# Performance work log

Measured on AMD Instinct MI355X. Metric: run time of the kernel, lower is better.

Reference implementation:

```python
import jax, jax.numpy as jnp
import numpy as np

B, M, N, P, H, W, D, DIMG, NH = 32, 2048, 512, 16, 640, 640, 256, 384, 8
PD = 3 * P * P  # 768 flattened patch dim


def layer_norm(x, g, b, eps=1e-5):
    mu = x.mean(-1, keepdims=True)
    var = ((x - mu) ** 2).mean(-1, keepdims=True)
    return (x - mu) * jax.lax.rsqrt(var + eps) * g + b


def get_patches(img, kpts, patch):
    # img [B,3,H,W], kpts [B,N,2] (x,y), NaN rows -> NaN patches
    Bb, C, Hh, Ww = img.shape
    half = patch // 2
    safe = jnp.nan_to_num(kpts, nan=0.0)
    ctr = jnp.round(safe).astype(jnp.int32)
    x0 = jnp.clip(ctr[..., 0] - half, 0, Ww - patch)
    y0 = jnp.clip(ctr[..., 1] - half, 0, Hh - patch)
    offs = jnp.arange(patch)
    ys = y0[..., None] + offs  # [B,N,P]
    xs = x0[..., None] + offs  # [B,N,P]

    def ext(im_b, ys_b, xs_b):
        p = im_b[:, ys_b[:, :, None], xs_b[:, None, :]]  # [C,N,P,P]
        return jnp.transpose(p, (1, 0, 2, 3))  # [N,C,P,P]

    patches = jax.vmap(ext)(img, ys, xs)  # [B,N,C,P,P]
    invalid = jnp.isnan(kpts).any(-1)
    return jnp.where(invalid[:, :, None, None, None], jnp.nan, patches)


def setup_inputs() -> dict:
    key = jax.random.key(0)
    ks = jax.random.split(key, 16)
    im0 = jax.random.uniform(ks[0], (B, 3, H, W), jnp.float32)
    im1 = jax.random.uniform(ks[1], (B, 3, H, W), jnp.float32)
    wh = jnp.array([W - 1.0, H - 1.0], jnp.float32)
    kpts0 = jax.random.uniform(ks[2], (B, M, 2), jnp.float32) * wh
    kpts1 = jax.random.uniform(ks[3], (B, M, 2), jnp.float32) * wh
    scores0 = jax.random.uniform(ks[4], (B, M), jnp.float32)
    scores1 = jax.random.uniform(ks[5], (B, M), jnp.float32)
    image_embs = jax.random.normal(ks[6], (B, DIMG), jnp.float32)
    m0 = jax.random.randint(ks[7], (B, N), 0, M)
    m1 = jax.random.randint(ks[8], (B, N), -300, M)
    m1 = jnp.where(m1 < 0, -1, m1)
    sorted_matches = jnp.stack([m0, m1], axis=-1).astype(jnp.int32)
    s = 0.02
    params = dict(
        ln1_g=jnp.ones((PD,), jnp.float32), ln1_b=jnp.zeros((PD,), jnp.float32),
        W_pe=jax.random.normal(ks[9], (D - 1, PD), jnp.float32) * s,
        b_pe=jnp.zeros((D - 1,), jnp.float32),
        ln2_g=jnp.ones((D - 1,), jnp.float32), ln2_b=jnp.zeros((D - 1,), jnp.float32),
        W_proj=jax.random.normal(ks[10], (D, DIMG), jnp.float32) * s,
        b_proj=jnp.zeros((D,), jnp.float32),
        in_w=jax.random.normal(ks[11], (3 * D, D), jnp.float32) * s,
        in_b=jnp.zeros((3 * D,), jnp.float32),
        out_w=jax.random.normal(ks[12], (D, D), jnp.float32) * s,
        out_b=jnp.zeros((D,), jnp.float32),
        W_fc=jax.random.normal(ks[13], (6, D), jnp.float32) * s,
        b_fc=jnp.zeros((6,), jnp.float32),
    )
    return dict(im0=im0, im1=im1, kpts0=kpts0, kpts1=kpts1, scores0=scores0,
                scores1=scores1, image_embs=image_embs,
                sorted_matches=sorted_matches, **params)


def reference(im0, im1, kpts0, kpts1, scores0, scores1, image_embs,
              sorted_matches, ln1_g, ln1_b, W_pe, b_pe, ln2_g, ln2_b,
              W_proj, b_proj, in_w, in_b, out_w, out_b, W_fc, b_fc):
    im0 = jnp.clip(im0, 0.0, 1.0)
    im1 = jnp.clip(im1, 0.0, 1.0)
    m0 = sorted_matches[..., 0]
    m1 = sorted_matches[..., 1]
    valid = m1 > -1  # [B,N]
    m0c = jnp.clip(m0, 0, M - 1)
    m1c = jnp.clip(m1, 0, M - 1)
    # vectorized masked gather with NaN padding (replaces the double python loop)
    g0 = jnp.take_along_axis(kpts0, m0c[..., None], axis=1)  # [B,N,2]
    g1 = jnp.take_along_axis(kpts1, m1c[..., None], axis=1)
    k0v = jnp.where(valid[..., None], g0, jnp.nan)
    k1v = jnp.where(valid[..., None], g1, jnp.nan)
    s0v = jnp.where(valid, jnp.take_along_axis(scores0, m0c, axis=1), 0.0)
    s1v = jnp.where(valid, jnp.take_along_axis(scores1, m1c, axis=1), 0.0)
    p0 = jnp.nan_to_num(get_patches(im0, k0v, P), nan=-1.0)  # [B,N,3,P,P]
    p1 = jnp.nan_to_num(get_patches(im1, k1v, P), nan=-1.0)
    patches = jnp.concatenate([p0, p1], axis=1)  # [B,2N,3,P,P]
    flat = patches.reshape(B, 2 * N, PD)
    e = layer_norm(flat, ln1_g, ln1_b)
    e = e @ W_pe.T + b_pe
    e = layer_norm(e, ln2_g, ln2_b)  # [B,2N,D-1]
    scores = jnp.concatenate([s0v, s1v], axis=1)  # [B,2N]
    pe = jnp.concatenate([e, scores[..., None]], axis=-1)  # [B,2N,D]
    # motion estimator: cross-attn, query = projected image embedding
    q = image_embs @ W_proj.T + b_proj  # [B,D]
    Wq, Wk, Wv = in_w[:D], in_w[D:2 * D], in_w[2 * D:]
    bq, bk, bv = in_b[:D], in_b[D:2 * D], in_b[2 * D:]
    dh = D // NH
    qh = (q @ Wq.T + bq).reshape(B, 1, NH, dh)
    kh = (pe @ Wk.T + bk).reshape(B, 2 * N, NH, dh)
    vh = (pe @ Wv.T + bv).reshape(B, 2 * N, NH, dh)
    scale = 1.0 / np.sqrt(dh).astype(np.float32)
    att = jnp.einsum('bqhd,bkhd->bhqk', qh, kh) * scale
    a = jax.nn.softmax(att, axis=-1)
    o = jnp.einsum('bhqk,bkhd->bqhd', a, vh).reshape(B, 1, D)
    o = o @ out_w.T + out_b
    out = (o @ W_fc.T + b_fc).reshape(B, 6)
    return out
```

## Files before the change

kernel.cpp:

```cpp
#include <hip/hip_runtime.h>
#include <math.h>

#define BB 32
#define MM 2048
#define NN 512
#define PSZ 16
#define HH 640
#define WW 640
#define DD 256
#define DIMG_ 384
#define NHEADS 8
#define PD_ 768
#define TWO_N 1024
#define ROWS_TOT (BB * TWO_N)

typedef short bf16x8 __attribute__((ext_vector_type(8)));
typedef float f32x4  __attribute__((ext_vector_type(4)));

__device__ __forceinline__ unsigned short f2bf(float x) {
  unsigned int u = __float_as_uint(x);
  u = (u + 0x7FFF + ((u >> 16) & 1)) >> 16;
  return (unsigned short)u;
}
__device__ __forceinline__ float bf2f(unsigned short h) {
  return __uint_as_float(((unsigned int)h) << 16);
}

__device__ __forceinline__ void gload_lds16(const void* g, void* l) {
  __builtin_amdgcn_global_load_lds(
      (const __attribute__((address_space(1))) void*)g,
      (__attribute__((address_space(3))) void*)l, 16, 0, 0);
}

__global__ __launch_bounds__(256) void prep_kernel(
    const float* __restrict__ W_pe,
    unsigned short* __restrict__ Whi, unsigned short* __restrict__ Wlo,
    const float* __restrict__ image_embs,
    const float* __restrict__ W_proj, const float* __restrict__ b_proj,
    const float* __restrict__ in_w,   const float* __restrict__ in_b,
    float* __restrict__ u_out, float* __restrict__ bias_out)
{
  __shared__ float q1[DD];
  __shared__ float q2[DD];
  const int t = threadIdx.x;

  if (blockIdx.x < 768) {
    const int idx = blockIdx.x * 256 + t;
    const int row = idx / PD_;
    float v = (row < 255) ? W_pe[idx] : 0.0f;
    const unsigned short h = f2bf(v);
    Whi[idx] = h;
    Wlo[idx] = f2bf(v - bf2f(h));
    return;
  }

  const int b = blockIdx.x - 768;
  {
    const float4* emb = (const float4*)(image_embs + (size_t)b * DIMG_);
    const float4* wr  = (const float4*)(W_proj + (size_t)t * DIMG_);
    float a = b_proj[t];
    #pragma unroll 4
    for (int i = 0; i < DIMG_ / 4; ++i) {
      const float4 e4 = emb[i], w4 = wr[i];
      a += e4.x * w4.x + e4.y * w4.y + e4.z * w4.z + e4.w * w4.w;
    }
    q1[t] = a;
  }
  __syncthreads();
  {
    const float4* wr = (const float4*)(in_w + (size_t)t * DD);
    const float4* qq = (const float4*)q1;
    float a = in_b[t];
    #pragma unroll 4
    for (int i = 0; i < DD / 4; ++i) {
      const float4 q4 = qq[i], w4 = wr[i];
      a += q4.x * w4.x + q4.y * w4.y + q4.z * w4.z + q4.w * w4.w;
    }
    q2[t] = a;
  }
  __syncthreads();
  #pragma unroll
  for (int h = 0; h < NHEADS; ++h) {
    float s = 0.0f;
    #pragma unroll 8
    for (int i = 0; i < 32; ++i)
      s += q2[h * 32 + i] * in_w[(size_t)(DD + h * 32 + i) * DD + t];
    u_out[((size_t)b * NHEADS + h) * DD + t] = s;
  }
  if (t < NHEADS) {
    float s = 0.0f;
    for (int i = 0; i < 32; ++i) s += q2[t * 32 + i] * in_b[DD + t * 32 + i];
    bias_out[b * NHEADS + t] = s;
  }
}

__global__ __launch_bounds__(256) void extract_kernel(
    const float* __restrict__ im0, const float* __restrict__ im1,
    const float* __restrict__ kpts0, const float* __restrict__ kpts1,
    const float* __restrict__ scores0, const float* __restrict__ scores1,
    const int*   __restrict__ sorted_matches,
    const float* __restrict__ ln1_g, const float* __restrict__ ln1_b,
    unsigned short* __restrict__ Ahi, unsigned short* __restrict__ Alo,
    float* __restrict__ score_all)
{
  const int t  = threadIdx.x;
  const int L  = t & 63;
  const long gp = (long)blockIdx.x * 4 + (t >> 6);
  const int b   = (int)(gp >> 10);
  const int n2  = (int)(gp & 1023);
  const bool side1 = (n2 >= NN);
  const float* img  = side1 ? im1 : im0;
  const float* kpts = side1 ? kpts1 : kpts0;
  const float* scrs = side1 ? scores1 : scores0;

  const int n  = side1 ? (n2 - NN) : n2;
  const int m0 = sorted_matches[((size_t)b * NN + n) * 2 + 0];
  const int m1 = sorted_matches[((size_t)b * NN + n) * 2 + 1];
  const bool valid = (m1 > -1);
  int midx = side1 ? m1 : m0;
  midx = min(max(midx, 0), MM - 1);
  const float kx = kpts[((size_t)b * MM + midx) * 2 + 0];
  const float ky = kpts[((size_t)b * MM + midx) * 2 + 1];
  const int x0 = min(max((int)rintf(kx) - 8, 0), WW - PSZ);
  const int y0 = min(max((int)rintf(ky) - 8, 0), HH - PSZ);

  float v[12];
  if (valid) {
    const size_t imb = (size_t)b * 3 * HH * WW;
    const int px = (2 * L) & 15;
    #pragma unroll
    for (int j = 0; j < 6; ++j) {
      const int p0 = 2 * L + 128 * j;
      const int c  = p0 >> 8;
      const int py = (p0 >> 4) & 15;
      const float* rp = img + imb + ((size_t)c * HH + y0 + py) * WW + x0 + px;
      v[2 * j]     = fminf(fmaxf(rp[0], 0.0f), 1.0f);
      v[2 * j + 1] = fminf(fmaxf(rp[1], 0.0f), 1.0f);
    }
  } else {
    #pragma unroll
    for (int i = 0; i < 12; ++i) v[i] = -1.0f;
  }

  float s = 0.0f, ss = 0.0f;
  #pragma unroll
  for (int i = 0; i < 12; ++i) { s += v[i]; ss += v[i] * v[i]; }
  #pragma unroll
  for (int m = 32; m; m >>= 1) { s += __shfl_xor(s, m); ss += __shfl_xor(ss, m); }
  const float mu  = s * (1.0f / 768.0f);
  const float var = ss * (1.0f / 768.0f) - mu * mu;
  const float rs  = 1.0f / sqrtf(var + 1e-5f);

  unsigned int* AhiW = (unsigned int*)(Ahi + gp * PD_);
  unsigned int* AloW = (unsigned int*)(Alo + gp * PD_);
  #pragma unroll
  for (int j = 0; j < 6; ++j) {
    const int p0 = 2 * L + 128 * j;
    const float y0e = (v[2 * j]     - mu) * rs * ln1_g[p0]     + ln1_b[p0];
    const float y1e = (v[2 * j + 1] - mu) * rs * ln1_g[p0 + 1] + ln1_b[p0 + 1];
    const unsigned short h0 = f2bf(y0e), h1 = f2bf(y1e);
    AhiW[p0 >> 1] = (unsigned int)h0 | ((unsigned int)h1 << 16);
    const unsigned short l0 = f2bf(y0e - bf2f(h0));
    const unsigned short l1 = f2bf(y1e - bf2f(h1));
    AloW[p0 >> 1] = (unsigned int)l0 | ((unsigned int)l1 << 16);
  }
  if (L == 0) {
    score_all[gp] = valid ? scrs[(size_t)b * MM + midx] : 0.0f;
  }
}

__global__ __launch_bounds__(256) void gemm_pe_kernel(
    const unsigned short* __restrict__ Ahi, const unsigned short* __restrict__ Alo,
    const unsigned short* __restrict__ Whi, const unsigned short* __restrict__ Wlo,
    float* __restrict__ e)
{
  __shared__ __align__(16) unsigned short As[2][128][32];
  __shared__ __align__(16) unsigned short Bs[2][128][32];

  const int t  = threadIdx.x;
  const int w  = t >> 6;
  const int L  = t & 63;
  const int id = blockIdx.x;
  const int nt = (id >> 3) & 1;
  const int mt = ((id >> 4) << 3) | (id & 7);

  f32x4 acc[4][4];
  #pragma unroll
  for (int i = 0; i < 4; ++i)
    #pragma unroll
    for (int j = 0; j < 4; ++j) acc[i][j] = (f32x4){0.f, 0.f, 0.f, 0.f};

  const unsigned short* src;
  unsigned short* dstbase;
  long rowbase;
  if      (w == 0) { src = Ahi; dstbase = &As[0][0][0]; rowbase = (long)mt * 128; }
  else if (w == 1) { src = Alo; dstbase = &As[1][0][0]; rowbase = (long)mt * 128; }
  else if (w == 2) { src = Whi; dstbase = &Bs[0][0][0]; rowbase = (long)nt * 128; }
  else             { src = Wlo; dstbase = &Bs[1][0][0]; rowbase = (long)nt * 128; }
  const int rr   = L >> 2;
  const int q_st = (L & 3) ^ ((L >> 4) & 3);

  const int lane_m = L & 15;
  const int quad   = L >> 4;
  const int swz    = quad ^ (lane_m >> 2);

  const unsigned short* As0 = &As[0][0][0];
  const unsigned short* As1 = &As[1][0][0];
  const unsigned short* Bs0 = &Bs[0][0][0];
  const unsigned short* Bs1 = &Bs[1][0][0];
  const int am0 = (w >> 1) * 64;
  const int bn0 = (w & 1) * 64;

  for (int ks = 0; ks < PD_ / 32; ++ks) {
    const int k0 = ks * 32;
    __syncthreads();
    {
      const unsigned short* gs = src + (rowbase + rr) * (long)PD_ + k0 + q_st * 8;
      #pragma unroll
      for (int c = 0; c < 8; ++c)
        gload_lds16(gs + (long)c * 16 * PD_, dstbase + c * 512);
    }
    __syncthreads();

    bf16x8 ah[4], al[4], bh[4], bl[4];
    #pragma unroll
    for (int i = 0; i < 4; ++i) {
      const int offa = (am0 + i * 16 + lane_m) * 32 + swz * 8;
      ah[i] = *(const bf16x8*)(As0 + offa);
      al[i] = *(const bf16x8*)(As1 + offa);
      const int offb = (bn0 + i * 16 + lane_m) * 32 + swz * 8;
      bh[i] = *(const bf16x8*)(Bs0 + offb);
      bl[i] = *(const bf16x8*)(Bs1 + offb);
    }
    #pragma unroll
    for (int i = 0; i < 4; ++i)
      #pragma unroll
      for (int j = 0; j < 4; ++j) {
        acc[i][j] = __builtin_amdgcn_mfma_f32_16x16x32_bf16(ah[i], bh[j], acc[i][j], 0, 0, 0);
        acc[i][j] = __builtin_amdgcn_mfma_f32_16x16x32_bf16(ah[i], bl[j], acc[i][j], 0, 0, 0);
        acc[i][j] = __builtin_amdgcn_mfma_f32_16x16x32_bf16(al[i], bh[j], acc[i][j], 0, 0, 0);
      }
  }

  const long grow0 = (long)mt * 128 + am0;
  const int  gcol0 = nt * 128 + bn0;
  #pragma unroll
  for (int i = 0; i < 4; ++i)
    #pragma unroll
    for (int j = 0; j < 4; ++j)
      #pragma unroll
      for (int v = 0; v < 4; ++v) {
        const long row = grow0 + i * 16 + quad * 4 + v;
        const int  col = gcol0 + j * 16 + lane_m;
        e[row * DD + col] = acc[i][j][v];
      }
}

__global__ __launch_bounds__(256) void ln2_logits_kernel(
    float* epe,
    const float* __restrict__ b_pe,
    const float* __restrict__ ln2_g, const float* __restrict__ ln2_b,
    const float* __restrict__ score_all,
    const float* __restrict__ u, const float* __restrict__ ubias,
    float* __restrict__ lt)
{
  const int t = threadIdx.x;
  const int g = t >> 5, l = t & 31;
  const long row = (long)blockIdx.x * 8 + g;
  const int  b   = (int)(row >> 10);
  float* er = epe + row * DD;

  float x[8];
  float s = 0.0f, ss = 0.0f;
  #pragma unroll
  for (int j = 0; j < 8; ++j) {
    const int c = l + 32 * j;
    float v = er[c];
    if (c < 255) { v += b_pe[c]; s += v; ss += v * v; }
    x[j] = v;
  }
  #pragma unroll
  for (int m = 16; m; m >>= 1) { s += __shfl_xor(s, m, 32); ss += __shfl_xor(ss, m, 32); }
  const float mu  = s * (1.0f / 255.0f);
  const float var = ss * (1.0f / 255.0f) - mu * mu;
  const float rs  = 1.0f / sqrtf(var + 1e-5f);

  float y[8];
  #pragma unroll
  for (int j = 0; j < 8; ++j) {
    const int c = l + 32 * j;
    y[j] = (c < 255) ? (x[j] - mu) * rs * ln2_g[c] + ln2_b[c] : score_all[row];
    er[c] = y[j];
  }

  const float* ub = u + (size_t)b * NHEADS * DD;
  float d[NHEADS] = {0, 0, 0, 0, 0, 0, 0, 0};
  #pragma unroll
  for (int j = 0; j < 8; ++j) {
    const int c = l + 32 * j;
    #pragma unroll
    for (int h = 0; h < NHEADS; ++h) d[h] += y[j] * ub[h * DD + c];
  }
  #pragma unroll
  for (int h = 0; h < NHEADS; ++h) {
    #pragma unroll
    for (int m = 16; m; m >>= 1) d[h] += __shfl_xor(d[h], m, 32);
  }
  if (l == 0) {
    const float sc = 0.17677669529663687f;
    #pragma unroll
    for (int h = 0; h < NHEADS; ++h)
      lt[row * NHEADS + h] = (d[h] + ubias[b * NHEADS + h]) * sc;
  }
}

__global__ __launch_bounds__(256) void ctx_kernel(
    const float* __restrict__ pe, const float* __restrict__ lt,
    float* __restrict__ ctxp)
{
  __shared__ __align__(16) float pr[TWO_N][NHEADS];
  const int b = blockIdx.x, ch = blockIdx.y, t = threadIdx.x;

  {
    const int h = t >> 5, l = t & 31;
    const float* base = lt + (size_t)b * TWO_N * NHEADS + h;
    float v[32];
    float mx = -1e30f;
    #pragma unroll 8
    for (int i = 0; i < 32; ++i) { v[i] = base[(l + 32 * i) * NHEADS]; mx = fmaxf(mx, v[i]); }
    #pragma unroll
    for (int m = 16; m; m >>= 1) mx = fmaxf(mx, __shfl_xor(mx, m, 32));
    float sm = 0.0f;
    #pragma unroll 8
    for (int i = 0; i < 32; ++i) { v[i] = expf(v[i] - mx); sm += v[i]; }
    #pragma unroll
    for (int m = 16; m; m >>= 1) sm += __shfl_xor(sm, m, 32);
    const float inv = 1.0f / sm;
    #pragma unroll 8
    for (int i = 0; i < 32; ++i) pr[l + 32 * i][h] = v[i] * inv;
  }
  __syncthreads();

  const float* peb = pe + ((size_t)b * TWO_N + ch * 128) * DD;
  float acc[NHEADS] = {0, 0, 0, 0, 0, 0, 0, 0};
  for (int k = 0; k < 128; ++k) {
    const float v = peb[(size_t)k * DD + t];
    const float4 a0 = *(const float4*)&pr[ch * 128 + k][0];
    const float4 a1 = *(const float4*)&pr[ch * 128 + k][4];
    acc[0] += a0.x * v; acc[1] += a0.y * v; acc[2] += a0.z * v; acc[3] += a0.w * v;
    acc[4] += a1.x * v; acc[5] += a1.y * v; acc[6] += a1.z * v; acc[7] += a1.w * v;
  }
  #pragma unroll
  for (int h = 0; h < NHEADS; ++h)
    ctxp[(((size_t)b * 8 + ch) * NHEADS + h) * DD + t] = acc[h];
}

__global__ __launch_bounds__(256) void final_kernel(
    const float* __restrict__ ctxp,
    const float* __restrict__ in_w,  const float* __restrict__ in_b,
    const float* __restrict__ out_w, const float* __restrict__ out_b,
    const float* __restrict__ W_fc,  const float* __restrict__ b_fc,
    float* __restrict__ outp)
{
  __shared__ __align__(16) float ctx_sh[NHEADS * DD];
  __shared__ __align__(16) float o_sh[DD], o2_sh[DD];
  const int t = threadIdx.x;
  const int b = blockIdx.x;

  #pragma unroll
  for (int h = 0; h < NHEADS; ++h) {
    float s = 0.0f;
    #pragma unroll
    for (int ch = 0; ch < 8; ++ch)
      s += ctxp[(((size_t)b * 8 + ch) * NHEADS + h) * DD + t];
    ctx_sh[h * DD + t] = s;
  }
  __syncthreads();
  {
    const float4* wv = (const float4*)(in_w + (size_t)(2 * DD + t) * DD);
    const float4* cx = (const float4*)(ctx_sh + (t >> 5) * DD);
    float o1 = in_b[2 * DD + t];
    #pragma unroll 4
    for (int j = 0; j < DD / 4; ++j) {
      const float4 w4 = wv[j], c4 = cx[j];
      o1 += w4.x * c4.x + w4.y * c4.y + w4.z * c4.z + w4.w * c4.w;
    }
    o_sh[t] = o1;
  }
  __syncthreads();
  {
    const float4* wr = (const float4*)(out_w + (size_t)t * DD);
    const float4* oo = (const float4*)o_sh;
    float o2 = out_b[t];
    #pragma unroll 4
    for (int j = 0; j < DD / 4; ++j) {
      const float4 w4 = wr[j], c4 = oo[j];
      o2 += w4.x * c4.x + w4.y * c4.y + w4.z * c4.z + w4.w * c4.w;
    }
    o2_sh[t] = o2;
  }
  __syncthreads();
  if (t < 6) {
    const float4* wr = (const float4*)(W_fc + (size_t)t * DD);
    const float4* oo = (const float4*)o2_sh;
    float r = b_fc[t];
    for (int j = 0; j < DD / 4; ++j) {
      const float4 w4 = wr[j], c4 = oo[j];
      r += w4.x * c4.x + w4.y * c4.y + w4.z * c4.z + w4.w * c4.w;
    }
    outp[b * 6 + t] = r;
  }
}

extern "C" void kernel_launch(void* const* d_in, const int* in_sizes, int n_in,
                              void* d_out, int out_size, void* d_ws, size_t ws_size,
                              hipStream_t stream) {
  const float* im0       = (const float*)d_in[0];
  const float* im1       = (const float*)d_in[1];
  const float* kpts0     = (const float*)d_in[2];
  const float* kpts1     = (const float*)d_in[3];
  const float* scores0   = (const float*)d_in[4];
  const float* scores1   = (const float*)d_in[5];
  const float* image_embs= (const float*)d_in[6];
  const int*   smatch    = (const int*)d_in[7];
  const float* ln1_g     = (const float*)d_in[8];
  const float* ln1_b     = (const float*)d_in[9];
  const float* W_pe      = (const float*)d_in[10];
  const float* b_pe      = (const float*)d_in[11];
  const float* ln2_g     = (const float*)d_in[12];
  const float* ln2_b     = (const float*)d_in[13];
  const float* W_proj    = (const float*)d_in[14];
  const float* b_proj    = (const float*)d_in[15];
  const float* in_w      = (const float*)d_in[16];
  const float* in_b      = (const float*)d_in[17];
  const float* out_w     = (const float*)d_in[18];
  const float* out_b     = (const float*)d_in[19];
  const float* W_fc      = (const float*)d_in[20];
  const float* b_fc      = (const float*)d_in[21];

  char* ws = (char*)d_ws;
  size_t off = 0;
  float* epe   = (float*)(ws + off); off += (size_t)ROWS_TOT * DD * 4;
  float* u     = (float*)(ws + off); off += (size_t)BB * NHEADS * DD * 4;
  float* ubias = (float*)(ws + off); off += (size_t)BB * NHEADS * 4;
  off = (off + 1023) & ~(size_t)1023;
  float* score = (float*)(ws + off); off += (size_t)ROWS_TOT * 4;
  float* lt    = (float*)(ws + off); off += (size_t)BB * TWO_N * NHEADS * 4;
  float* ctxp  = (float*)(ws + off); off += (size_t)BB * 8 * NHEADS * DD * 4;
  unsigned short* Whi = (unsigned short*)(ws + off); off += (size_t)256 * PD_ * 2;
  unsigned short* Wlo = (unsigned short*)(ws + off); off += (size_t)256 * PD_ * 2;
  off = (off + 1023) & ~(size_t)1023;
  unsigned short* Ahi = (unsigned short*)(ws + off); off += (size_t)ROWS_TOT * PD_ * 2;
  unsigned short* Alo = (unsigned short*)(ws + off); off += (size_t)ROWS_TOT * PD_ * 2;

  prep_kernel<<<768 + BB, 256, 0, stream>>>(W_pe, Whi, Wlo,
                                            image_embs, W_proj, b_proj,
                                            in_w, in_b, u, ubias);
  extract_kernel<<<ROWS_TOT / 4, 256, 0, stream>>>(
      im0, im1, kpts0, kpts1, scores0, scores1, smatch,
      ln1_g, ln1_b, Ahi, Alo, score);
  gemm_pe_kernel<<<(ROWS_TOT / 128) * 2, 256, 0, stream>>>(Ahi, Alo, Whi, Wlo, epe);
  ln2_logits_kernel<<<ROWS_TOT / 8, 256, 0, stream>>>(
      epe, b_pe, ln2_g, ln2_b, score, u, ubias, lt);
  ctx_kernel<<<dim3(BB, 8), 256, 0, stream>>>(epe, lt, ctxp);
  final_kernel<<<BB, 256, 0, stream>>>(ctxp, in_w, in_b, out_w, out_b,
                                       W_fc, b_fc, (float*)d_out);
}
```

Baseline: 498.8 us.

## Fuse LN2 and logits into double-buffered full-width GEMM, merge prep and extract

```diff
diff --git a/kernel.cpp b/kernel.cpp
--- a/kernel.cpp
+++ b/kernel.cpp
@@ -13,6 +13,7 @@
 #define PD_ 768
 #define TWO_N 1024
 #define ROWS_TOT (BB * TWO_N)
+#define CHCT 16
 
 typedef short bf16x8 __attribute__((ext_vector_type(8)));
 typedef float f32x4  __attribute__((ext_vector_type(4)));
@@ -32,13 +33,20 @@
       (__attribute__((address_space(3))) void*)l, 16, 0, 0);
 }
 
-__global__ __launch_bounds__(256) void prep_kernel(
+__global__ __launch_bounds__(256) void prep_extract_kernel(
     const float* __restrict__ W_pe,
     unsigned short* __restrict__ Whi, unsigned short* __restrict__ Wlo,
     const float* __restrict__ image_embs,
     const float* __restrict__ W_proj, const float* __restrict__ b_proj,
     const float* __restrict__ in_w,   const float* __restrict__ in_b,
-    float* __restrict__ u_out, float* __restrict__ bias_out)
+    float* __restrict__ u_out, float* __restrict__ bias_out,
+    const float* __restrict__ im0, const float* __restrict__ im1,
+    const float* __restrict__ kpts0, const float* __restrict__ kpts1,
+    const float* __restrict__ scores0, const float* __restrict__ scores1,
+    const int*   __restrict__ sorted_matches,
+    const float* __restrict__ ln1_g, const float* __restrict__ ln1_b,
+    unsigned short* __restrict__ Ahi, unsigned short* __restrict__ Alo,
+    float* __restrict__ score_all)
 {
   __shared__ float q1[DD];
   __shared__ float q2[DD];
@@ -54,58 +62,50 @@
     return;
   }
 
-  const int b = blockIdx.x - 768;
-  {
-    const float4* emb = (const float4*)(image_embs + (size_t)b * DIMG_);
-    const float4* wr  = (const float4*)(W_proj + (size_t)t * DIMG_);
-    float a = b_proj[t];
-    #pragma unroll 4
-    for (int i = 0; i < DIMG_ / 4; ++i) {
-      const float4 e4 = emb[i], w4 = wr[i];
-      a += e4.x * w4.x + e4.y * w4.y + e4.z * w4.z + e4.w * w4.w;
-    }
-    q1[t] = a;
-  }
-  __syncthreads();
-  {
-    const float4* wr = (const float4*)(in_w + (size_t)t * DD);
-    const float4* qq = (const float4*)q1;
-    float a = in_b[t];
-    #pragma unroll 4
-    for (int i = 0; i < DD / 4; ++i) {
-      const float4 q4 = qq[i], w4 = wr[i];
-      a += q4.x * w4.x + q4.y * w4.y + q4.z * w4.z + q4.w * w4.w;
-    }
-    q2[t] = a;
-  }
-  __syncthreads();
-  #pragma unroll
-  for (int h = 0; h < NHEADS; ++h) {
-    float s = 0.0f;
-    #pragma unroll 8
-    for (int i = 0; i < 32; ++i)
-      s += q2[h * 32 + i] * in_w[(size_t)(DD + h * 32 + i) * DD + t];
-    u_out[((size_t)b * NHEADS + h) * DD + t] = s;
-  }
-  if (t < NHEADS) {
-    float s = 0.0f;
-    for (int i = 0; i < 32; ++i) s += q2[t * 32 + i] * in_b[DD + t * 32 + i];
-    bias_out[b * NHEADS + t] = s;
-  }
-}
-
-__global__ __launch_bounds__(256) void extract_kernel(
-    const float* __restrict__ im0, const float* __restrict__ im1,
-    const float* __restrict__ kpts0, const float* __restrict__ kpts1,
-    const float* __restrict__ scores0, const float* __restrict__ scores1,
-    const int*   __restrict__ sorted_matches,
-    const float* __restrict__ ln1_g, const float* __restrict__ ln1_b,
-    unsigned short* __restrict__ Ahi, unsigned short* __restrict__ Alo,
-    float* __restrict__ score_all)
-{
-  const int t  = threadIdx.x;
+  if (blockIdx.x < 800) {
+    const int b = blockIdx.x - 768;
+    {
+      const float4* emb = (const float4*)(image_embs + (size_t)b * DIMG_);
+      const float4* wr  = (const float4*)(W_proj + (size_t)t * DIMG_);
+      float a = b_proj[t];
+      #pragma unroll 4
+      for (int i = 0; i < DIMG_ / 4; ++i) {
+        const float4 e4 = emb[i], w4 = wr[i];
+        a += e4.x * w4.x + e4.y * w4.y + e4.z * w4.z + e4.w * w4.w;
+      }
+      q1[t] = a;
+    }
+    __syncthreads();
+    {
+      const float4* wr = (const float4*)(in_w + (size_t)t * DD);
+      const float4* qq = (const float4*)q1;
+      float a = in_b[t];
+      #pragma unroll 4
+      for (int i = 0; i < DD / 4; ++i) {
+        const float4 q4 = qq[i], w4 = wr[i];
+        a += q4.x * w4.x + q4.y * w4.y + q4.z * w4.z + q4.w * w4.w;
+      }
+      q2[t] = a;
+    }
+    __syncthreads();
+    #pragma unroll
+    for (int h = 0; h < NHEADS; ++h) {
+      float s = 0.0f;
+      #pragma unroll 8
+      for (int i = 0; i < 32; ++i)
+        s += q2[h * 32 + i] * in_w[(size_t)(DD + h * 32 + i) * DD + t];
+      u_out[((size_t)b * NHEADS + h) * DD + t] = s;
+    }
+    if (t < NHEADS) {
+      float s = 0.0f;
+      for (int i = 0; i < 32; ++i) s += q2[t * 32 + i] * in_b[DD + t * 32 + i];
+      bias_out[b * NHEADS + t] = s;
+    }
+    return;
+  }
+
   const int L  = t & 63;
-  const long gp = (long)blockIdx.x * 4 + (t >> 6);
+  const long gp = (long)(blockIdx.x - 800) * 4 + (t >> 6);
   const int b   = (int)(gp >> 10);
   const int n2  = (int)(gp & 1023);
   const bool side1 = (n2 >= NN);
@@ -169,68 +169,99 @@
   }
 }
 
-__global__ __launch_bounds__(256) void gemm_pe_kernel(
+__global__ __launch_bounds__(512, 1) void gemm_fused_kernel(
     const unsigned short* __restrict__ Ahi, const unsigned short* __restrict__ Alo,
     const unsigned short* __restrict__ Whi, const unsigned short* __restrict__ Wlo,
-    float* __restrict__ e)
+    const float* __restrict__ b_pe,
+    const float* __restrict__ ln2_g, const float* __restrict__ ln2_b,
+    const float* __restrict__ score_all,
+    const float* __restrict__ u, const float* __restrict__ ubias,
+    float* __restrict__ pe, float* __restrict__ lt)
 {
-  __shared__ __align__(16) unsigned short As[2][128][32];
-  __shared__ __align__(16) unsigned short Bs[2][128][32];
-
-  const int t  = threadIdx.x;
-  const int w  = t >> 6;
-  const int L  = t & 63;
-  const int id = blockIdx.x;
-  const int nt = (id >> 3) & 1;
-  const int mt = ((id >> 4) << 3) | (id & 7);
-
-  f32x4 acc[4][4];
-  #pragma unroll
-  for (int i = 0; i < 4; ++i)
-    #pragma unroll
-    for (int j = 0; j < 4; ++j) acc[i][j] = (f32x4){0.f, 0.f, 0.f, 0.f};
-
-  const unsigned short* src;
-  unsigned short* dstbase;
-  long rowbase;
-  if      (w == 0) { src = Ahi; dstbase = &As[0][0][0]; rowbase = (long)mt * 128; }
-  else if (w == 1) { src = Alo; dstbase = &As[1][0][0]; rowbase = (long)mt * 128; }
-  else if (w == 2) { src = Whi; dstbase = &Bs[0][0][0]; rowbase = (long)nt * 128; }
-  else             { src = Wlo; dstbase = &Bs[1][0][0]; rowbase = (long)nt * 128; }
+  __shared__ __align__(16) char smem[98304];
+  __shared__ float u_lds[NHEADS * DD];
+  __shared__ float cv_bpe[DD], cv_g[DD], cv_b[DD];
+  __shared__ float ub_lds[NHEADS];
+
+  unsigned short* const sbase = (unsigned short*)smem;
+  const int t = threadIdx.x;
+  const int w = t >> 6, L = t & 63;
+  const int mt = blockIdx.x;
+  const int bidx = mt >> 3;
+
+  {
+    const float* ub0 = u + (size_t)bidx * NHEADS * DD;
+    #pragma unroll
+    for (int i = 0; i < 4; ++i) u_lds[t + 512 * i] = ub0[t + 512 * i];
+    if (t < DD) {
+      cv_bpe[t] = (t < 255) ? b_pe[t]  : 0.0f;
+      cv_g[t]   = (t < 255) ? ln2_g[t] : 0.0f;
+      cv_b[t]   = (t < 255) ? ln2_b[t] : 0.0f;
+    }
+    if (t < NHEADS) ub_lds[t] = ubias[bidx * NHEADS + t];
+  }
+
   const int rr   = L >> 2;
   const int q_st = (L & 3) ^ ((L >> 4) & 3);
 
-  const int lane_m = L & 15;
-  const int quad   = L >> 4;
-  const int swz    = quad ^ (lane_m >> 2);
-
-  const unsigned short* As0 = &As[0][0][0];
-  const unsigned short* As1 = &As[1][0][0];
-  const unsigned short* Bs0 = &Bs[0][0][0];
-  const unsigned short* Bs1 = &Bs[1][0][0];
-  const int am0 = (w >> 1) * 64;
-  const int bn0 = (w & 1) * 64;
+  const unsigned short* gsrc[6];
+  int loff0[6], sstr[6];
+  #pragma unroll
+  for (int c = 0; c < 6; ++c) {
+    const int cc = w * 6 + c;
+    const unsigned short* sp; long row; int off, str;
+    if (cc < 16) {
+      sp  = (cc < 8) ? Ahi : Alo;
+      row = (long)mt * 128 + (cc & 7) * 16 + rr;
+      off = ((cc >> 3) * 128 + (cc & 7) * 16) * 32;
+      str = 8192;
+    } else {
+      const int c2 = cc - 16;
+      sp  = (c2 < 16) ? Whi : Wlo;
+      row = (c2 & 15) * 16 + rr;
+      off = 16384 + ((c2 >> 4) * 256 + (c2 & 15) * 16) * 32;
+      str = 16384;
+    }
+    gsrc[c]  = sp + row * (long)PD_ + q_st * 8;
+    loff0[c] = off;
+    sstr[c]  = str;
+  }
+
+  const int lane_m = L & 15, quad = L >> 4;
+  const int swz = quad ^ (lane_m >> 2);
+  const int wr = w >> 2, wc = w & 3;
+  const int am0 = wr * 64, bn0 = wc * 64;
+
+  f32x4 acc[4][4];
+  #pragma unroll
+  for (int i = 0; i < 4; ++i)
+    #pragma unroll
+    for (int j = 0; j < 4; ++j) acc[i][j] = (f32x4){0.f, 0.f, 0.f, 0.f};
+
+  #pragma unroll
+  for (int c = 0; c < 6; ++c) gload_lds16(gsrc[c], sbase + loff0[c]);
+  __syncthreads();
 
   for (int ks = 0; ks < PD_ / 32; ++ks) {
-    const int k0 = ks * 32;
-    __syncthreads();
-    {
-      const unsigned short* gs = src + (rowbase + rr) * (long)PD_ + k0 + q_st * 8;
+    const int cur = ks & 1;
+    if (ks < PD_ / 32 - 1) {
+      const int k0n = (ks + 1) * 32;
+      const int nb  = cur ^ 1;
       #pragma unroll
-      for (int c = 0; c < 8; ++c)
-        gload_lds16(gs + (long)c * 16 * PD_, dstbase + c * 512);
-    }
-    __syncthreads();
-
+      for (int c = 0; c < 6; ++c)
+        gload_lds16(gsrc[c] + k0n, sbase + loff0[c] + nb * sstr[c]);
+    }
+    const unsigned short* Ab = sbase + cur * 8192;
+    const unsigned short* Bb = sbase + 16384 + cur * 16384;
     bf16x8 ah[4], al[4], bh[4], bl[4];
     #pragma unroll
     for (int i = 0; i < 4; ++i) {
-      const int offa = (am0 + i * 16 + lane_m) * 32 + swz * 8;
-      ah[i] = *(const bf16x8*)(As0 + offa);
-      al[i] = *(const bf16x8*)(As1 + offa);
-      const int offb = (bn0 + i * 16 + lane_m) * 32 + swz * 8;
-      bh[i] = *(const bf16x8*)(Bs0 + offb);
-      bl[i] = *(const bf16x8*)(Bs1 + offb);
+      const int ra = (am0 + i * 16 + lane_m) * 32 + swz * 8;
+      ah[i] = *(const bf16x8*)(Ab + ra);
+      al[i] = *(const bf16x8*)(Ab + 4096 + ra);
+      const int rb = (bn0 + i * 16 + lane_m) * 32 + swz * 8;
+      bh[i] = *(const bf16x8*)(Bb + rb);
+      bl[i] = *(const bf16x8*)(Bb + 8192 + rb);
     }
     #pragma unroll
     for (int i = 0; i < 4; ++i)
@@ -240,77 +271,65 @@
         acc[i][j] = __builtin_amdgcn_mfma_f32_16x16x32_bf16(ah[i], bl[j], acc[i][j], 0, 0, 0);
         acc[i][j] = __builtin_amdgcn_mfma_f32_16x16x32_bf16(al[i], bh[j], acc[i][j], 0, 0, 0);
       }
-  }
-
-  const long grow0 = (long)mt * 128 + am0;
-  const int  gcol0 = nt * 128 + bn0;
-  #pragma unroll
-  for (int i = 0; i < 4; ++i)
-    #pragma unroll
-    for (int j = 0; j < 4; ++j)
+    __syncthreads();
+  }
+
+  float* const eb = (float*)smem;
+  const int r8 = t >> 3, l8 = t & 7;
+  #pragma unroll
+  for (int hh = 0; hh < 2; ++hh) {
+    if (hh) __syncthreads();
+    if (wr == hh) {
       #pragma unroll
-      for (int v = 0; v < 4; ++v) {
-        const long row = grow0 + i * 16 + quad * 4 + v;
-        const int  col = gcol0 + j * 16 + lane_m;
-        e[row * DD + col] = acc[i][j][v];
-      }
-}
-
-__global__ __launch_bounds__(256) void ln2_logits_kernel(
-    float* epe,
-    const float* __restrict__ b_pe,
-    const float* __restrict__ ln2_g, const float* __restrict__ ln2_b,
-    const float* __restrict__ score_all,
-    const float* __restrict__ u, const float* __restrict__ ubias,
-    float* __restrict__ lt)
-{
-  const int t = threadIdx.x;
-  const int g = t >> 5, l = t & 31;
-  const long row = (long)blockIdx.x * 8 + g;
-  const int  b   = (int)(row >> 10);
-  float* er = epe + row * DD;
-
-  float x[8];
-  float s = 0.0f, ss = 0.0f;
-  #pragma unroll
-  for (int j = 0; j < 8; ++j) {
-    const int c = l + 32 * j;
-    float v = er[c];
-    if (c < 255) { v += b_pe[c]; s += v; ss += v * v; }
-    x[j] = v;
-  }
-  #pragma unroll
-  for (int m = 16; m; m >>= 1) { s += __shfl_xor(s, m, 32); ss += __shfl_xor(ss, m, 32); }
-  const float mu  = s * (1.0f / 255.0f);
-  const float var = ss * (1.0f / 255.0f) - mu * mu;
-  const float rs  = 1.0f / sqrtf(var + 1e-5f);
-
-  float y[8];
-  #pragma unroll
-  for (int j = 0; j < 8; ++j) {
-    const int c = l + 32 * j;
-    y[j] = (c < 255) ? (x[j] - mu) * rs * ln2_g[c] + ln2_b[c] : score_all[row];
-    er[c] = y[j];
-  }
-
-  const float* ub = u + (size_t)b * NHEADS * DD;
-  float d[NHEADS] = {0, 0, 0, 0, 0, 0, 0, 0};
-  #pragma unroll
-  for (int j = 0; j < 8; ++j) {
-    const int c = l + 32 * j;
-    #pragma unroll
-    for (int h = 0; h < NHEADS; ++h) d[h] += y[j] * ub[h * DD + c];
-  }
-  #pragma unroll
-  for (int h = 0; h < NHEADS; ++h) {
-    #pragma unroll
-    for (int m = 16; m; m >>= 1) d[h] += __shfl_xor(d[h], m, 32);
-  }
-  if (l == 0) {
-    const float sc = 0.17677669529663687f;
-    #pragma unroll
-    for (int h = 0; h < NHEADS; ++h)
-      lt[row * NHEADS + h] = (d[h] + ubias[b * NHEADS + h]) * sc;
+      for (int i = 0; i < 4; ++i)
+        #pragma unroll
+        for (int j = 0; j < 4; ++j)
+          #pragma unroll
+          for (int v = 0; v < 4; ++v)
+            eb[(i * 16 + quad * 4 + v) * 260 + bn0 + j * 16 + lane_m] = acc[i][j][v];
+    }
+    __syncthreads();
+
+    const long grow = (long)mt * 128 + hh * 64 + r8;
+    float x[32];
+    float s = 0.0f, ss = 0.0f;
+    #pragma unroll
+    for (int j = 0; j < 32; ++j) {
+      const int c = l8 + 8 * j;
+      float vv = eb[r8 * 260 + c];
+      if (c < 255) { vv += cv_bpe[c]; s += vv; ss += vv * vv; }
+      x[j] = vv;
+    }
+    s += __shfl_xor(s, 1); ss += __shfl_xor(ss, 1);
+    s += __shfl_xor(s, 2); ss += __shfl_xor(ss, 2);
+    s += __shfl_xor(s, 4); ss += __shfl_xor(ss, 4);
+    const float mu  = s * (1.0f / 255.0f);
+    const float var = ss * (1.0f / 255.0f) - mu * mu;
+    const float rs  = 1.0f / sqrtf(var + 1e-5f);
+
+    float scrow = 0.0f;
+    if (l8 == 7) scrow = score_all[grow];
+
+    float d[NHEADS] = {0, 0, 0, 0, 0, 0, 0, 0};
+    float* const per = pe + grow * DD;
+    #pragma unroll
+    for (int j = 0; j < 32; ++j) {
+      const int c = l8 + 8 * j;
+      const float y = (c < 255) ? (x[j] - mu) * rs * cv_g[c] + cv_b[c] : scrow;
+      per[c] = y;
+      #pragma unroll
+      for (int h = 0; h < NHEADS; ++h) d[h] += y * u_lds[h * DD + c];
+    }
+    #pragma unroll
+    for (int h = 0; h < NHEADS; ++h) {
+      d[h] += __shfl_xor(d[h], 1);
+      d[h] += __shfl_xor(d[h], 2);
+      d[h] += __shfl_xor(d[h], 4);
+    }
+    const float dv = (l8 == 0) ? d[0] : (l8 == 1) ? d[1] : (l8 == 2) ? d[2] :
+                     (l8 == 3) ? d[3] : (l8 == 4) ? d[4] : (l8 == 5) ? d[5] :
+                     (l8 == 6) ? d[6] : d[7];
+    lt[grow * NHEADS + l8] = (dv + ub_lds[l8]) * 0.17677669529663687f;
   }
 }
 
@@ -341,18 +360,19 @@
   }
   __syncthreads();
 
-  const float* peb = pe + ((size_t)b * TWO_N + ch * 128) * DD;
+  const float* peb = pe + ((size_t)b * TWO_N + ch * 64) * DD;
   float acc[NHEADS] = {0, 0, 0, 0, 0, 0, 0, 0};
-  for (int k = 0; k < 128; ++k) {
+  #pragma unroll 4
+  for (int k = 0; k < 64; ++k) {
     const float v = peb[(size_t)k * DD + t];
-    const float4 a0 = *(const float4*)&pr[ch * 128 + k][0];
-    const float4 a1 = *(const float4*)&pr[ch * 128 + k][4];
+    const float4 a0 = *(const float4*)&pr[ch * 64 + k][0];
+    const float4 a1 = *(const float4*)&pr[ch * 64 + k][4];
     acc[0] += a0.x * v; acc[1] += a0.y * v; acc[2] += a0.z * v; acc[3] += a0.w * v;
     acc[4] += a1.x * v; acc[5] += a1.y * v; acc[6] += a1.z * v; acc[7] += a1.w * v;
   }
   #pragma unroll
   for (int h = 0; h < NHEADS; ++h)
-    ctxp[(((size_t)b * 8 + ch) * NHEADS + h) * DD + t] = acc[h];
+    ctxp[(((size_t)b * CHCT + ch) * NHEADS + h) * DD + t] = acc[h];
 }
 
 __global__ __launch_bounds__(256) void final_kernel(
@@ -371,8 +391,8 @@
   for (int h = 0; h < NHEADS; ++h) {
     float s = 0.0f;
     #pragma unroll
-    for (int ch = 0; ch < 8; ++ch)
-      s += ctxp[(((size_t)b * 8 + ch) * NHEADS + h) * DD + t];
+    for (int ch = 0; ch < CHCT; ++ch)
+      s += ctxp[(((size_t)b * CHCT + ch) * NHEADS + h) * DD + t];
     ctx_sh[h * DD + t] = s;
   }
   __syncthreads();
@@ -446,23 +466,20 @@
   off = (off + 1023) & ~(size_t)1023;
   float* score = (float*)(ws + off); off += (size_t)ROWS_TOT * 4;
   float* lt    = (float*)(ws + off); off += (size_t)BB * TWO_N * NHEADS * 4;
-  float* ctxp  = (float*)(ws + off); off += (size_t)BB * 8 * NHEADS * DD * 4;
+  float* ctxp  = (float*)(ws + off); off += (size_t)BB * CHCT * NHEADS * DD * 4;
   unsigned short* Whi = (unsigned short*)(ws + off); off += (size_t)256 * PD_ * 2;
   unsigned short* Wlo = (unsigned short*)(ws + off); off += (size_t)256 * PD_ * 2;
   off = (off + 1023) & ~(size_t)1023;
   unsigned short* Ahi = (unsigned short*)(ws + off); off += (size_t)ROWS_TOT * PD_ * 2;
   unsigned short* Alo = (unsigned short*)(ws + off); off += (size_t)ROWS_TOT * PD_ * 2;
 
-  prep_kernel<<<768 + BB, 256, 0, stream>>>(W_pe, Whi, Wlo,
-                                            image_embs, W_proj, b_proj,
-                                            in_w, in_b, u, ubias);
-  extract_kernel<<<ROWS_TOT / 4, 256, 0, stream>>>(
+  prep_extract_kernel<<<800 + ROWS_TOT / 4, 256, 0, stream>>>(
+      W_pe, Whi, Wlo, image_embs, W_proj, b_proj, in_w, in_b, u, ubias,
       im0, im1, kpts0, kpts1, scores0, scores1, smatch,
       ln1_g, ln1_b, Ahi, Alo, score);
-  gemm_pe_kernel<<<(ROWS_TOT / 128) * 2, 256, 0, stream>>>(Ahi, Alo, Whi, Wlo, epe);
-  ln2_logits_kernel<<<ROWS_TOT / 8, 256, 0, stream>>>(
-      epe, b_pe, ln2_g, ln2_b, score, u, ubias, lt);
-  ctx_kernel<<<dim3(BB, 8), 256, 0, stream>>>(epe, lt, ctxp);
+  gemm_fused_kernel<<<ROWS_TOT / 128, 512, 0, stream>>>(
+      Ahi, Alo, Whi, Wlo, b_pe, ln2_g, ln2_b, score, u, ubias, epe, lt);
+  ctx_kernel<<<dim3(BB, CHCT), 256, 0, stream>>>(epe, lt, ctxp);
   final_kernel<<<BB, 256, 0, stream>>>(ctxp, in_w, in_b, out_w, out_b,
                                        W_fc, b_fc, (float*)d_out);
 }
```

New measurement: 510.0 us. +2.2%, slower.
